# Performance work log

Hardware: AMD Instinct MI355X
Metric: run time of the kernel (lower is better)

## Reference

```python
import jax, jax.numpy as jnp
import numpy as np

B, D, H, E, K = 8192, 1024, 256, 16, 4


def setup_inputs() -> dict:
    key = jax.random.key(0)
    ks = jax.random.split(key, 6)
    s_d = D ** -0.5
    s_h = H ** -0.5
    return {
        "x": jax.random.normal(ks[0], (B, D), dtype=jnp.float32),
        "route_w": jax.random.normal(ks[1], (E, D), dtype=jnp.float32) * s_d,
        "w1": jax.random.normal(ks[2], (E, H, D), dtype=jnp.float32) * s_d,
        "b1": jax.random.normal(ks[3], (E, H), dtype=jnp.float32) * s_d,
        "w2": jax.random.normal(ks[4], (E, D, H), dtype=jnp.float32) * s_h,
        "b2": jax.random.normal(ks[5], (E, D), dtype=jnp.float32) * s_h,
    }


def _moe_forward(x, route_w, w1, b1, w2, b2):
    # Router: logits (B, E) -> top-k softmax weights scattered back to (B, E).
    logits = x @ route_w.T
    top_vals, top_idx = jax.lax.top_k(logits, K)
    top_w = jax.nn.softmax(top_vals, axis=-1)
    rows = jnp.arange(x.shape[0])[:, None]
    weights = jnp.zeros_like(logits).at[rows, top_idx].set(top_w)  # (B, E)

    # Experts: out = sum_e w[:, e] * relu(relu(x W1e^T + b1e) W2e^T + b2e)
    # Non-selected experts have weight 0, so dense-then-weight matches the
    # original masked gather/scatter math exactly (dropout = 0).
    def step(out, params_e):
        W1, bb1, W2, bb2, we = params_e
        h = jax.nn.relu(x @ W1.T + bb1)       # (B, H)
        y = jax.nn.relu(h @ W2.T + bb2)       # (B, D)
        return out + y * we[:, None], None

    out0 = jnp.zeros_like(x)
    out, _ = jax.lax.scan(step, out0, (w1, b1, w2, b2, weights.T))
    return out


def reference(x, route_w, w1, b1, w2, b2):
    return _moe_forward(x, route_w, w1, b1, w2, b2)
```

## Files before the change

### kernel.cpp

```cpp
#include <hip/hip_runtime.h>
#include <stdint.h>

typedef unsigned short u16;
typedef __attribute__((ext_vector_type(8))) short bf16x8;
typedef __attribute__((ext_vector_type(4))) float f32x4;
typedef __attribute__((ext_vector_type(8))) u16 u16x8;
typedef __attribute__((ext_vector_type(4))) u16 u16x4;

#define NTOK 8192
#define DDIM 1024
#define HDIM 256
#define NEXP 16
#define MAXT 272
#define MAXSLOT (MAXT * 128)

__device__ __forceinline__ u16 f2bf(float f) {
  uint32_t u = __builtin_bit_cast(uint32_t, f);
  u += 0x7FFFu + ((u >> 16) & 1u);
  return (u16)(u >> 16);
}
__device__ __forceinline__ float bf2f(u16 h) {
  return __builtin_bit_cast(float, (uint32_t)h << 16);
}

__device__ __forceinline__ void gll16(const void* g, void* l) {
  __builtin_amdgcn_global_load_lds((const __attribute__((address_space(1))) void*)g,
                                   (__attribute__((address_space(3))) void*)l,
                                   16, 0, 0);
}

__global__ __launch_bounds__(256) void cvt_kernel(const float* __restrict__ in,
                                                  u16* __restrict__ out) {
  size_t i = ((size_t)blockIdx.x * 256 + threadIdx.x) * 8;
  const float4 a = *(const float4*)(in + i);
  const float4 b = *(const float4*)(in + i + 4);
  u16x8 o;
  o[0] = f2bf(a.x); o[1] = f2bf(a.y); o[2] = f2bf(a.z); o[3] = f2bf(a.w);
  o[4] = f2bf(b.x); o[5] = f2bf(b.y); o[6] = f2bf(b.z); o[7] = f2bf(b.w);
  *(u16x8*)(out + i) = o;
}

__global__ __launch_bounds__(256) void zero_out_kernel(float* __restrict__ p) {
  size_t i = ((size_t)blockIdx.x * 256 + threadIdx.x) * 4;
  *(float4*)(p + i) = (float4){0.f, 0.f, 0.f, 0.f};
}

__global__ __launch_bounds__(256) void router_kernel(const float* __restrict__ x,
                                                     const float* __restrict__ rw,
                                                     int* __restrict__ epack,
                                                     float* __restrict__ ew,
                                                     u16* __restrict__ xbf) {
  const int wid = threadIdx.x >> 6, lane = threadIdx.x & 63;
  const int b = blockIdx.x * 4 + wid;
  double acc[NEXP];
#pragma unroll
  for (int e = 0; e < NEXP; ++e) acc[e] = 0.0;
#pragma unroll 4
  for (int i = 0; i < 16; ++i) {
    int d = lane + i * 64;
    float xv = x[(size_t)b * DDIM + d];
    xbf[(size_t)b * DDIM + d] = f2bf(xv);
#pragma unroll
    for (int e = 0; e < NEXP; ++e) acc[e] += (double)xv * (double)rw[e * DDIM + d];
  }
#pragma unroll
  for (int e = 0; e < NEXP; ++e) {
#pragma unroll
    for (int off = 32; off > 0; off >>= 1) acc[e] += __shfl_xor(acc[e], off);
  }
  if (lane == 0) {
    float v[NEXP];
#pragma unroll
    for (int e = 0; e < NEXP; ++e) v[e] = (float)acc[e];
    int idx[4]; float tv[4];
    unsigned used = 0;
    for (int k = 0; k < 4; ++k) {
      int bi = 0; float bv = -3.4e38f;
      for (int e = 0; e < NEXP; ++e)
        if (!((used >> e) & 1u) && v[e] > bv) { bv = v[e]; bi = e; }
      idx[k] = bi; tv[k] = bv; used |= 1u << bi;
    }
    float m = tv[0];
    float w[4]; float s = 0.f;
    for (int k = 0; k < 4; ++k) { w[k] = expf(tv[k] - m); s += w[k]; }
    epack[b] = idx[0] | (idx[1] << 8) | (idx[2] << 16) | (idx[3] << 24);
    for (int k = 0; k < 4; ++k) ew[b * 4 + k] = w[k] / s;
  }
}

__global__ __launch_bounds__(1024) void compact_kernel(const int* __restrict__ epack,
                                                       const float* __restrict__ ew,
                                                       int* __restrict__ texp,
                                                       int* __restrict__ perm,
                                                       float* __restrict__ wsl,
                                                       int* __restrict__ islot) {
  __shared__ int wave_cnt[16][NEXP];
  __shared__ int counts_sm[NEXP];
  __shared__ int wtot[16], wave_off[16];
  const int e = blockIdx.x;
  const int tid = threadIdx.x, lane = tid & 63, w = tid >> 6;

  int ep[8]; unsigned m[8];
#pragma unroll
  for (int j = 0; j < 8; ++j) {
    ep[j] = epack[tid * 8 + j];
    m[j] = (1u << (ep[j] & 255)) | (1u << ((ep[j] >> 8) & 255)) |
           (1u << ((ep[j] >> 16) & 255)) | (1u << ((ep[j] >> 24) & 255));
  }
#pragma unroll
  for (int ee = 0; ee < NEXP; ++ee) {
    int c = 0;
#pragma unroll
    for (int j = 0; j < 8; ++j) c += (m[j] >> ee) & 1u;
#pragma unroll
    for (int off = 32; off > 0; off >>= 1) c += __shfl_xor(c, off);
    if (lane == 0) wave_cnt[w][ee] = c;
  }
  unsigned fm = 0;
#pragma unroll
  for (int j = 0; j < 8; ++j) fm |= ((m[j] >> e) & 1u) << j;
  int s = __popc(fm);
  int incl = s;
#pragma unroll
  for (int d = 1; d < 64; d <<= 1) {
    int t2 = __shfl_up(incl, d);
    if (lane >= d) incl += t2;
  }
  if (lane == 63) wtot[w] = incl;
  __syncthreads();
  if (tid < NEXP) {
    int c = 0;
    for (int w2 = 0; w2 < 16; ++w2) c += wave_cnt[w2][tid];
    counts_sm[tid] = c;
  }
  if (tid == 0) {
    int run = 0;
    for (int w2 = 0; w2 < 16; ++w2) { wave_off[w2] = run; run += wtot[w2]; }
  }
  __syncthreads();
  int base = 0;
  for (int ee = 0; ee < NEXP; ++ee)
    if (ee < e) base += ((counts_sm[ee] + 127) >> 7) << 7;
  int pos = base + wave_off[w] + (incl - s);
#pragma unroll
  for (int j = 0; j < 8; ++j) {
    if ((fm >> j) & 1u) {
      int tok = tid * 8 + j;
      int b0 = ep[j] & 255, b1 = (ep[j] >> 8) & 255, b2_ = (ep[j] >> 16) & 255;
      int k = (b0 == e) ? 0 : ((b1 == e) ? 1 : ((b2_ == e) ? 2 : 3));
      perm[pos] = tok;
      wsl[pos] = ew[tok * 4 + k];
      islot[tok * 4 + k] = pos;
      ++pos;
    }
  }
  int cnt = counts_sm[e];
  int pad = (((cnt + 127) >> 7) << 7) - cnt;
  if (tid < pad) { perm[base + cnt + tid] = 0; wsl[base + cnt + tid] = 0.f; }
  if (e == 0 && tid == 0) {
    int tc = 0;
    for (int ee = 0; ee < NEXP; ++ee) {
      int nt = (counts_sm[ee] + 127) >> 7;
      for (int i = 0; i < nt; ++i) texp[tc++] = ee;
    }
    for (; tc < MAXT; ++tc) texp[tc] = -1;
  }
}

__device__ __forceinline__ void stage_rows(const u16* __restrict__ base, int ld,
                                           int kbase, uint8_t* dst, int tid) {
#pragma unroll
  for (int i = 0; i < 4; ++i) {
    int u = i * 256 + tid;
    int row = u >> 3, g = u & 7;
    gll16(base + (size_t)row * ld + kbase + ((g ^ (row & 7)) << 3), dst + u * 16);
  }
}
__device__ __forceinline__ void stage_gather(const u16* __restrict__ xbf,
                                             const int tok[4], int kbase,
                                             uint8_t* dst, int tid) {
#pragma unroll
  for (int i = 0; i < 4; ++i) {
    int u = i * 256 + tid;
    int row = u >> 3, g = u & 7;
    gll16(xbf + (size_t)tok[i] * DDIM + kbase + ((g ^ (row & 7)) << 3), dst + u * 16);
  }
}

__device__ __forceinline__ void mma_tile(const uint8_t* Ab, const uint8_t* Bb,
                                         f32x4 acc[4][4], int wm, int wn,
                                         int lrow, int lk) {
#pragma unroll
  for (int s = 0; s < 2; ++s) {
    bf16x8 af[4], bfr[4];
#pragma unroll
    for (int f = 0; f < 4; ++f) {
      int ar = wm * 64 + f * 16 + lrow;
      af[f] = *(const bf16x8*)(Ab + ar * 128 + ((((s << 2) | lk) ^ (ar & 7)) << 4));
      int br = wn * 64 + f * 16 + lrow;
      bfr[f] = *(const bf16x8*)(Bb + br * 128 + ((((s << 2) | lk) ^ (br & 7)) << 4));
    }
#pragma unroll
    for (int i = 0; i < 4; ++i)
#pragma unroll
      for (int j = 0; j < 4; ++j)
        acc[i][j] = __builtin_amdgcn_mfma_f32_16x16x32_bf16(af[i], bfr[j], acc[i][j], 0, 0, 0);
  }
}

__global__ __launch_bounds__(256) void gemm1_kernel(const u16* __restrict__ xbf,
                                                    const u16* __restrict__ w1bf,
                                                    const float* __restrict__ b1,
                                                    const int* __restrict__ texp,
                                                    const int* __restrict__ perm,
                                                    u16* __restrict__ Hc, int t0) {
  __shared__ __align__(16) uint8_t smem[2][32768];
  const int t = t0 + blockIdx.x;
  const int e = (t < MAXT) ? texp[t] : -1;
  if (e < 0) return;
  const int n0 = blockIdx.y * 128;
  const int tid = threadIdx.x;
  const int lane = tid & 63, wid = tid >> 6;
  const int wm = wid >> 1, wn = wid & 1;
  const int lrow = lane & 15, lk = lane >> 4;

  int tok[4];
#pragma unroll
  for (int i = 0; i < 4; ++i) tok[i] = perm[t * 128 + ((i * 256 + tid) >> 3)];
  const u16* Bsrc = w1bf + ((size_t)e * HDIM + n0) * DDIM;

  f32x4 acc[4][4];
#pragma unroll
  for (int i = 0; i < 4; ++i)
#pragma unroll
    for (int j = 0; j < 4; ++j) acc[i][j] = (f32x4){0.f, 0.f, 0.f, 0.f};

  stage_gather(xbf, tok, 0, smem[0], tid);
  stage_rows(Bsrc, DDIM, 0, smem[0] + 16384, tid);
  __syncthreads();
  int cur = 0;
  for (int kt = 0; kt < 16; ++kt) {
    if (kt < 15) {
      stage_gather(xbf, tok, (kt + 1) * 64, smem[cur ^ 1], tid);
      stage_rows(Bsrc, DDIM, (kt + 1) * 64, smem[cur ^ 1] + 16384, tid);
    }
    mma_tile(smem[cur], smem[cur] + 16384, acc, wm, wn, lrow, lk);
    __syncthreads();
    cur ^= 1;
  }
#pragma unroll
  for (int j = 0; j < 4; ++j) {
    int n = n0 + wn * 64 + j * 16 + lrow;
    float bias = b1[e * HDIM + n];
#pragma unroll
    for (int i = 0; i < 4; ++i) {
      int rloc = blockIdx.x * 128 + wm * 64 + i * 16 + lk * 4;
#pragma unroll
      for (int r = 0; r < 4; ++r) {
        float h = fmaxf(acc[i][j][r] + bias, 0.f);
        Hc[((size_t)rloc + r) * HDIM + n] = f2bf(h);
      }
    }
  }
}

template <int MODE>
__global__ __launch_bounds__(256) void gemm2_kernel(const u16* __restrict__ Hc,
                                                    const u16* __restrict__ w2bf,
                                                    const float* __restrict__ b2,
                                                    const int* __restrict__ texp,
                                                    const int* __restrict__ perm,
                                                    const float* __restrict__ wsl,
                                                    float* __restrict__ out,
                                                    u16* __restrict__ ybuf,
                                                    int t0, int n0, int NC) {
  __shared__ __align__(16) uint8_t smem[2][32768];
  const int t = t0 + blockIdx.x;
  const int e = (t < MAXT) ? texp[t] : -1;
  if (e < 0) return;
  const int tid = threadIdx.x;
  const int lane = tid & 63, wid = tid >> 6;
  const int wm = wid >> 1, wn = wid & 1;
  const int lrow = lane & 15, lk = lane >> 4;

  const u16* Asrc = Hc + (size_t)blockIdx.x * 128 * HDIM;
  const u16* Bsrc = w2bf + ((size_t)e * DDIM + n0 + blockIdx.y * 128) * HDIM;

  f32x4 acc[4][4];
#pragma unroll
  for (int i = 0; i < 4; ++i)
#pragma unroll
    for (int j = 0; j < 4; ++j) acc[i][j] = (f32x4){0.f, 0.f, 0.f, 0.f};

  stage_rows(Asrc, HDIM, 0, smem[0], tid);
  stage_rows(Bsrc, HDIM, 0, smem[0] + 16384, tid);
  __syncthreads();
  int cur = 0;
  for (int kt = 0; kt < 4; ++kt) {
    if (kt < 3) {
      stage_rows(Asrc, HDIM, (kt + 1) * 64, smem[cur ^ 1], tid);
      stage_rows(Bsrc, HDIM, (kt + 1) * 64, smem[cur ^ 1] + 16384, tid);
    }
    mma_tile(smem[cur], smem[cur] + 16384, acc, wm, wn, lrow, lk);
    __syncthreads();
    cur ^= 1;
  }
  float bias[4];
#pragma unroll
  for (int j = 0; j < 4; ++j)
    bias[j] = b2[e * DDIM + n0 + blockIdx.y * 128 + wn * 64 + j * 16 + lrow];
#pragma unroll
  for (int i = 0; i < 4; ++i) {
#pragma unroll
    for (int r = 0; r < 4; ++r) {
      int slot = t * 128 + wm * 64 + i * 16 + lk * 4 + r;
      if (MODE == 0) {
        int tokn = perm[slot];
        float w = wsl[slot];
#pragma unroll
        for (int j = 0; j < 4; ++j) {
          int n = n0 + blockIdx.y * 128 + wn * 64 + j * 16 + lrow;
          float h = fmaxf(acc[i][j][r] + bias[j], 0.f);
          atomicAdd(&out[(size_t)tokn * DDIM + n], w * h);
        }
      } else {
#pragma unroll
        for (int j = 0; j < 4; ++j) {
          int nloc = blockIdx.y * 128 + wn * 64 + j * 16 + lrow;
          float h = fmaxf(acc[i][j][r] + bias[j], 0.f);
          ybuf[(size_t)slot * NC + nloc] = f2bf(h);
        }
      }
    }
  }
}

__global__ __launch_bounds__(256) void combine_kernel(const u16* __restrict__ ybuf,
                                                      const float* __restrict__ ew,
                                                      const int* __restrict__ islot,
                                                      float* __restrict__ out,
                                                      int n0, int NC, int cshift) {
  int gid = blockIdx.x * 256 + threadIdx.x;
  int t = gid >> cshift;
  int c = (gid & ((1 << cshift) - 1)) << 2;
  const int4 sl = *(const int4*)(islot + t * 4);
  const float4 w = *(const float4*)(ew + t * 4);
  float4 a = {0.f, 0.f, 0.f, 0.f};
#define ACC(SL, W)                                             \
  {                                                            \
    u16x4 y = *(const u16x4*)(ybuf + (size_t)(SL)*NC + c);     \
    a.x += (W)*bf2f(y[0]); a.y += (W)*bf2f(y[1]);              \
    a.z += (W)*bf2f(y[2]); a.w += (W)*bf2f(y[3]);              \
  }
  ACC(sl.x, w.x); ACC(sl.y, w.y); ACC(sl.z, w.z); ACC(sl.w, w.w);
#undef ACC
  *(float4*)(out + (size_t)t * DDIM + n0 + c) = a;
}

extern "C" void kernel_launch(void* const* d_in, const int* in_sizes, int n_in,
                              void* d_out, int out_size, void* d_ws, size_t ws_size,
                              hipStream_t stream) {
  const float* x = (const float*)d_in[0];
  const float* route_w = (const float*)d_in[1];
  const float* w1 = (const float*)d_in[2];
  const float* b1 = (const float*)d_in[3];
  const float* w2 = (const float*)d_in[4];
  const float* b2 = (const float*)d_in[5];
  float* out = (float*)d_out;

  uint8_t* ws = (uint8_t*)d_ws;
  const size_t OFF_EPACK = 0;
  const size_t OFF_EW    = 32768;
  const size_t OFF_ISLOT = 163840;
  const size_t OFF_TEXP  = 294912;
  const size_t OFF_PERM  = 296960;
  const size_t OFF_WSL   = 436224;
  const size_t OFF_X     = 1048576;
  const size_t OFF_W1    = OFF_X + (size_t)NTOK * DDIM * 2;
  const size_t OFF_W2    = OFF_W1 + (size_t)NEXP * HDIM * DDIM * 2;
  const size_t OFF_HC    = OFF_W2 + (size_t)NEXP * DDIM * HDIM * 2;
  const size_t OFF_Y     = OFF_HC + (size_t)MAXSLOT * HDIM * 2;

  int* epack  = (int*)(ws + OFF_EPACK);
  float* ew   = (float*)(ws + OFF_EW);
  int* islot  = (int*)(ws + OFF_ISLOT);
  int* texp   = (int*)(ws + OFF_TEXP);
  int* perm   = (int*)(ws + OFF_PERM);
  float* wsl  = (float*)(ws + OFF_WSL);
  u16* xbf    = (u16*)(ws + OFF_X);
  u16* w1bf   = (u16*)(ws + OFF_W1);
  u16* w2bf   = (u16*)(ws + OFF_W2);
  u16* Hc     = (u16*)(ws + OFF_HC);
  u16* ybuf   = (u16*)(ws + OFF_Y);

  cvt_kernel<<<dim3((NEXP * HDIM * DDIM) / 2048), 256, 0, stream>>>(w1, w1bf);
  cvt_kernel<<<dim3((NEXP * DDIM * HDIM) / 2048), 256, 0, stream>>>(w2, w2bf);
  router_kernel<<<dim3(NTOK / 4), 256, 0, stream>>>(x, route_w, epack, ew, xbf);
  compact_kernel<<<dim3(NEXP), 1024, 0, stream>>>(epack, ew, texp, perm, wsl, islot);

  int NC = 0;
  for (int cand = 1024; cand >= 128; cand >>= 1) {
    if (ws_size >= OFF_Y + (size_t)MAXSLOT * cand * 2) { NC = cand; break; }
  }

  if (NC > 0 && ws_size >= OFF_Y) {
    gemm1_kernel<<<dim3(MAXT, HDIM / 128), 256, 0, stream>>>(xbf, w1bf, b1, texp, perm, Hc, 0);
    int cshift = __builtin_ctz(NC >> 2);
    for (int n0 = 0; n0 < DDIM; n0 += NC) {
      gemm2_kernel<1><<<dim3(MAXT, NC / 128), 256, 0, stream>>>(
          Hc, w2bf, b2, texp, perm, wsl, out, ybuf, 0, n0, NC);
      combine_kernel<<<dim3((NTOK << cshift) / 256), 256, 0, stream>>>(
          ybuf, ew, islot, out, n0, NC, cshift);
    }
  } else {
    long room = (long)ws_size - (long)OFF_HC;
    int CT = (int)(room / 65536);
    if (CT > MAXT) CT = MAXT;
    if (CT < 16) CT = 16;
    zero_out_kernel<<<dim3((NTOK * DDIM) / 1024), 256, 0, stream>>>(out);
    for (int t0 = 0; t0 < MAXT; t0 += CT) {
      int ct = (MAXT - t0 < CT) ? (MAXT - t0) : CT;
      gemm1_kernel<<<dim3(ct, HDIM / 128), 256, 0, stream>>>(xbf, w1bf, b1, texp, perm, Hc, t0);
      gemm2_kernel<0><<<dim3(ct, DDIM / 128), 256, 0, stream>>>(
          Hc, w2bf, b2, texp, perm, wsl, out, ybuf, t0, 0, DDIM);
    }
  }
}
```

Measured before the change: 154.2 us.

## Vectorize router loads, pre-convert route weights to double, wave-parallel top-k

Adds a small kernel that converts route_w to double once, so the router reads it with vectorized f64 loads instead of converting per element. Tokens are read as float4 and written to bf16 in 4-wide chunks. The 16 per-expert reductions become a butterfly fold that leaves one expert per lane, and top-4 selection runs in parallel across lanes with shuffles instead of serially on lane 0. This cuts router instruction count and shuffle traffic at the cost of one extra tiny launch and doubled route-weight bytes.

```diff
diff --git a/kernel.cpp b/kernel.cpp
--- a/kernel.cpp
+++ b/kernel.cpp
@@ -6,6 +6,7 @@
 typedef __attribute__((ext_vector_type(4))) float f32x4;
 typedef __attribute__((ext_vector_type(8))) u16 u16x8;
 typedef __attribute__((ext_vector_type(4))) u16 u16x4;
+typedef __attribute__((ext_vector_type(2))) double f64x2;
 
 #define NTOK 8192
 #define DDIM 1024
@@ -45,45 +46,83 @@
   *(float4*)(p + i) = (float4){0.f, 0.f, 0.f, 0.f};
 }
 
+__global__ __launch_bounds__(256) void rwd_kernel(const float* __restrict__ rw,
+                                                  double* __restrict__ rwd) {
+  int i = blockIdx.x * 256 + threadIdx.x;
+  rwd[i] = (double)rw[i];
+}
+
 __global__ __launch_bounds__(256) void router_kernel(const float* __restrict__ x,
-                                                     const float* __restrict__ rw,
+                                                     const double* __restrict__ rwd,
                                                      int* __restrict__ epack,
                                                      float* __restrict__ ew,
                                                      u16* __restrict__ xbf) {
   const int wid = threadIdx.x >> 6, lane = threadIdx.x & 63;
   const int b = blockIdx.x * 4 + wid;
+  const float* xrow = x + (size_t)b * DDIM;
+
   double acc[NEXP];
 #pragma unroll
   for (int e = 0; e < NEXP; ++e) acc[e] = 0.0;
-#pragma unroll 4
-  for (int i = 0; i < 16; ++i) {
-    int d = lane + i * 64;
-    float xv = x[(size_t)b * DDIM + d];
-    xbf[(size_t)b * DDIM + d] = f2bf(xv);
-#pragma unroll
-    for (int e = 0; e < NEXP; ++e) acc[e] += (double)xv * (double)rw[e * DDIM + d];
-  }
-#pragma unroll
-  for (int e = 0; e < NEXP; ++e) {
-#pragma unroll
-    for (int off = 32; off > 0; off >>= 1) acc[e] += __shfl_xor(acc[e], off);
-  }
+
+#pragma unroll
+  for (int i = 0; i < 4; ++i) {
+    const int d = lane * 4 + i * 256;
+    float4 xv = *(const float4*)(xrow + d);
+    u16x4 o;
+    o[0] = f2bf(xv.x); o[1] = f2bf(xv.y); o[2] = f2bf(xv.z); o[3] = f2bf(xv.w);
+    *(u16x4*)(xbf + (size_t)b * DDIM + d) = o;
+    const double x0 = xv.x, x1 = xv.y, x2 = xv.z, x3 = xv.w;
+#pragma unroll
+    for (int e = 0; e < NEXP; ++e) {
+      const double* rp = rwd + e * DDIM + d;
+      f64x2 r0 = *(const f64x2*)rp;
+      f64x2 r1 = *(const f64x2*)(rp + 2);
+      acc[e] = fma(x0, r0[0], acc[e]);
+      acc[e] = fma(x1, r0[1], acc[e]);
+      acc[e] = fma(x2, r1[0], acc[e]);
+      acc[e] = fma(x3, r1[1], acc[e]);
+    }
+  }
+
+#define FOLD(H, M)                                                   \
+  _Pragma("unroll") for (int i = 0; i < H; ++i) {                    \
+    double send = (lane & M) ? acc[i] : acc[i + H];                  \
+    double recv = __shfl_xor(send, M);                               \
+    acc[i] = ((lane & M) ? acc[i + H] : acc[i]) + recv;              \
+  }
+  FOLD(8, 1)
+  FOLD(4, 2)
+  FOLD(2, 4)
+  FOLD(1, 8)
+#undef FOLD
+  acc[0] += __shfl_xor(acc[0], 16);
+  acc[0] += __shfl_xor(acc[0], 32);
+  const int e_mine = ((lane & 1) << 3) | ((lane & 2) << 1) |
+                     ((lane & 4) >> 1) | ((lane & 8) >> 3);
+
+  double val = acc[0];
+  double tv[4]; int tidx[4];
+#pragma unroll
+  for (int k = 0; k < 4; ++k) {
+    double bv = val; int be = e_mine;
+#pragma unroll
+    for (int m = 1; m < 16; m <<= 1) {
+      double ov = __shfl_xor(bv, m);
+      int oe = __shfl_xor(be, m);
+      if (ov > bv || (ov == bv && oe < be)) { bv = ov; be = oe; }
+    }
+    tv[k] = bv; tidx[k] = be;
+    if (e_mine == be) val = -1.0e300;
+  }
+
   if (lane == 0) {
-    float v[NEXP];
-#pragma unroll
-    for (int e = 0; e < NEXP; ++e) v[e] = (float)acc[e];
-    int idx[4]; float tv[4];
-    unsigned used = 0;
-    for (int k = 0; k < 4; ++k) {
-      int bi = 0; float bv = -3.4e38f;
-      for (int e = 0; e < NEXP; ++e)
-        if (!((used >> e) & 1u) && v[e] > bv) { bv = v[e]; bi = e; }
-      idx[k] = bi; tv[k] = bv; used |= 1u << bi;
-    }
-    float m = tv[0];
+    float m0 = (float)tv[0];
     float w[4]; float s = 0.f;
-    for (int k = 0; k < 4; ++k) { w[k] = expf(tv[k] - m); s += w[k]; }
-    epack[b] = idx[0] | (idx[1] << 8) | (idx[2] << 16) | (idx[3] << 24);
+#pragma unroll
+    for (int k = 0; k < 4; ++k) { w[k] = expf((float)tv[k] - m0); s += w[k]; }
+    epack[b] = tidx[0] | (tidx[1] << 8) | (tidx[2] << 16) | (tidx[3] << 24);
+#pragma unroll
     for (int k = 0; k < 4; ++k) ew[b * 4 + k] = w[k] / s;
   }
 }
@@ -375,6 +414,7 @@
   const size_t OFF_TEXP  = 294912;
   const size_t OFF_PERM  = 296960;
   const size_t OFF_WSL   = 436224;
+  const size_t OFF_RWD   = 786432;
   const size_t OFF_X     = 1048576;
   const size_t OFF_W1    = OFF_X + (size_t)NTOK * DDIM * 2;
   const size_t OFF_W2    = OFF_W1 + (size_t)NEXP * HDIM * DDIM * 2;
@@ -387,15 +427,17 @@
   int* texp   = (int*)(ws + OFF_TEXP);
   int* perm   = (int*)(ws + OFF_PERM);
   float* wsl  = (float*)(ws + OFF_WSL);
+  double* rwd = (double*)(ws + OFF_RWD);
   u16* xbf    = (u16*)(ws + OFF_X);
   u16* w1bf   = (u16*)(ws + OFF_W1);
   u16* w2bf   = (u16*)(ws + OFF_W2);
   u16* Hc     = (u16*)(ws + OFF_HC);
   u16* ybuf   = (u16*)(ws + OFF_Y);
 
+  rwd_kernel<<<dim3((NEXP * DDIM) / 256), 256, 0, stream>>>(route_w, rwd);
   cvt_kernel<<<dim3((NEXP * HDIM * DDIM) / 2048), 256, 0, stream>>>(w1, w1bf);
   cvt_kernel<<<dim3((NEXP * DDIM * HDIM) / 2048), 256, 0, stream>>>(w2, w2bf);
-  router_kernel<<<dim3(NTOK / 4), 256, 0, stream>>>(x, route_w, epack, ew, xbf);
+  router_kernel<<<dim3(NTOK / 4), 256, 0, stream>>>(x, rwd, epack, ew, xbf);
   compact_kernel<<<dim3(NEXP), 1024, 0, stream>>>(epack, ew, texp, perm, wsl, islot);
 
   int NC = 0;
@@ -403,7 +445,7 @@
     if (ws_size >= OFF_Y + (size_t)MAXSLOT * cand * 2) { NC = cand; break; }
   }
 
-  if (NC > 0 && ws_size >= OFF_Y) {
+  if (NC > 0) {
     gemm1_kernel<<<dim3(MAXT, HDIM / 128), 256, 0, stream>>>(xbf, w1bf, b1, texp, perm, Hc, 0);
     int cshift = __builtin_ctz(NC >> 2);
     for (int n0 = 0; n0 < DDIM; n0 += NC) {
```

Result: slower. 169.1 us (+9.6%).
